# Performance work log

Measured on AMD Instinct MI355X. Metric: run time of the kernel, lower is better.

The kernel has to match this reference:

```python
import jax, jax.numpy as jnp
import numpy as np

INPUT_SIZE = 128
HIDDEN_SIZE = 128
BATCH = 65536


def _xavier(key, shape):
    fan_out, fan_in = shape
    limit = np.sqrt(6.0 / (fan_in + fan_out)).astype(np.float32)
    return jax.random.uniform(key, shape, jnp.float32, -limit, limit)


def setup_inputs() -> dict:
    key = jax.random.key(0)
    ks = jax.random.split(key, 12)
    inp = {
        "x": jax.random.normal(ks[0], (BATCH, INPUT_SIZE), jnp.float32),
        "h_t": jax.random.normal(ks[1], (BATCH, HIDDEN_SIZE), jnp.float32),
        "c_t": jax.random.normal(ks[2], (BATCH, HIDDEN_SIZE), jnp.float32),
        "W_ii": _xavier(ks[3], (HIDDEN_SIZE, INPUT_SIZE)),
        "W_hi": _xavier(ks[4], (HIDDEN_SIZE, HIDDEN_SIZE)),
        "b_i": jnp.zeros((HIDDEN_SIZE,), jnp.float32),
        "W_if": _xavier(ks[5], (HIDDEN_SIZE, INPUT_SIZE)),
        "W_hf": _xavier(ks[6], (HIDDEN_SIZE, HIDDEN_SIZE)),
        "b_f": jnp.zeros((HIDDEN_SIZE,), jnp.float32),
        "W_ig": _xavier(ks[7], (HIDDEN_SIZE, INPUT_SIZE)),
        "W_hg": _xavier(ks[8], (HIDDEN_SIZE, HIDDEN_SIZE)),
        "b_g": jnp.zeros((HIDDEN_SIZE,), jnp.float32),
        "W_io": _xavier(ks[9], (HIDDEN_SIZE, INPUT_SIZE)),
        "W_ho": _xavier(ks[10], (HIDDEN_SIZE, HIDDEN_SIZE)),
        "b_o": jnp.zeros((HIDDEN_SIZE,), jnp.float32),
    }
    return inp


def reference(x, h_t, c_t, W_ii, W_hi, b_i, W_if, W_hf, b_f, W_ig, W_hg, b_g, W_io, W_ho, b_o):
    # Fuse the 8 small GEMMs into 2 concatenated GEMMs, identical math to
    # per-gate F.linear calls (same weights, just stacked along output dim).
    W_x = jnp.concatenate([W_ii, W_if, W_ig, W_io], axis=0)   # [4H, I]
    W_h = jnp.concatenate([W_hi, W_hf, W_hg, W_ho], axis=0)   # [4H, H]
    b = jnp.concatenate([b_i, b_f, b_g, b_o], axis=0)         # [4H]
    gates = x @ W_x.T + h_t @ W_h.T + b                       # [B, 4H]
    i_a, f_a, g_a, o_a = jnp.split(gates, 4, axis=1)
    i_t = jax.nn.sigmoid(i_a)
    f_t = jax.nn.sigmoid(f_a)
    g_t = jnp.tanh(g_a)
    o_t = jax.nn.sigmoid(o_a)
    c_new = f_t * c_t + i_t * g_t
    h_new = o_t * jnp.tanh(c_new)
    return (h_new, c_new)
```

## Files before the change

kernel.cpp:

```cpp
#include <hip/hip_runtime.h>
#include <hip/hip_bf16.h>


typedef short s16x8 __attribute__((ext_vector_type(8)));
typedef float f32x4 __attribute__((ext_vector_type(4)));

__device__ __forceinline__ short f2bf(float f) {
    __hip_bfloat16 h = __float2bfloat16(f);
    return __builtin_bit_cast(short, h);
}
__device__ __forceinline__ float sigm(float x) { return 1.0f / (1.0f + __expf(-x)); }
__device__ __forceinline__ float tanh_f(float x) { return 1.0f - 2.0f / (1.0f + __expf(2.0f * x)); }

__global__ __launch_bounds__(256)
void repack_weights(const float* __restrict__ Wii, const float* __restrict__ Whi,
                    const float* __restrict__ Wif, const float* __restrict__ Whf,
                    const float* __restrict__ Wig, const float* __restrict__ Whg,
                    const float* __restrict__ Wio, const float* __restrict__ Who,
                    short* __restrict__ ws)
{
    const int t     = blockIdx.x * 256 + threadIdx.x;
    const int chunk = t >> 6;
    const int l     = t & 63;
    const int ks    = chunk & 3;
    const int half  = (chunk >> 2) & 1;
    const int g     = (chunk >> 3) & 3;
    const int wn    = (chunk >> 5) & 1;
    const int jt    = chunk >> 6;
    const int j     = jt * 32 + wn * 16 + (l & 15);
    const int k0    = (ks * 4 + (l >> 4)) * 8;

    const float* wp;
    if (half == 0) wp = (g == 0) ? Wii : (g == 1) ? Wif : (g == 2) ? Wig : Wio;
    else           wp = (g == 0) ? Whi : (g == 1) ? Whf : (g == 2) ? Whg : Who;

    const float* src = wp + (size_t)j * 128 + k0;
    f32x4 a = *(const f32x4*)src;
    f32x4 b = *(const f32x4*)(src + 4);
    s16x8 v;
#pragma unroll
    for (int k = 0; k < 4; ++k) { v[k] = f2bf(a[k]); v[4 + k] = f2bf(b[k]); }
    *(s16x8*)(ws + (size_t)t * 8) = v;
}

__global__ __launch_bounds__(256, 3)
void lstm_cell_kernel(const float* __restrict__ X,
                      const float* __restrict__ H,
                      const float* __restrict__ C,
                      const float* __restrict__ Bi, const float* __restrict__ Bf,
                      const float* __restrict__ Bg, const float* __restrict__ Bo,
                      const short* __restrict__ WS,
                      float* __restrict__ OutH,
                      float* __restrict__ OutC)
{
    __shared__ short sA[128 * 128];

    const int tid = threadIdx.x;
    const int l  = tid & 63;
    const int w  = tid >> 6;
    const int wm = w & 1;
    const int wn = w >> 1;
    const int lj = l & 15;
    const int lq = l >> 4;

    const int jt = blockIdx.x & 3;
    const int bb = blockIdx.x >> 2;
    const int B0 = bb * 128;
    const int J0 = jt * 32;

    f32x4 acc[4][4];
#pragma unroll
    for (int mt = 0; mt < 4; ++mt)
#pragma unroll
        for (int g = 0; g < 4; ++g)
            acc[mt][g] = (f32x4){0.f, 0.f, 0.f, 0.f};

    const short* wsbase = WS + ((size_t)(jt * 2 + wn) * 32) * 512 + l * 8;

#pragma unroll
    for (int half = 0; half < 2; ++half) {
        const float* Asrc = half ? H : X;

        s16x8 bfh[4][4];
#pragma unroll
        for (int g = 0; g < 4; ++g)
#pragma unroll
            for (int ks = 0; ks < 4; ++ks)
                bfh[g][ks] = *(const s16x8*)(wsbase + (size_t)((g * 2 + half) * 4 + ks) * 512);

#pragma unroll
        for (int tt = 0; tt < 2; ++tt) {
            f32x4 f[4][2];
#pragma unroll
            for (int t = 0; t < 4; ++t) {
                const int cc   = (tt * 4 + t) * 256 + tid;
                const int m    = cc >> 4;
                const int oct  = cc & 15;
                const int soct = oct ^ (m & 15);
                const float* src = Asrc + (size_t)(B0 + m) * 128 + soct * 8;
                f[t][0] = *(const f32x4*)src;
                f[t][1] = *(const f32x4*)(src + 4);
            }
#pragma unroll
            for (int t = 0; t < 4; ++t) {
                const int cc = (tt * 4 + t) * 256 + tid;
                s16x8 v;
#pragma unroll
                for (int k = 0; k < 4; ++k) {
                    v[k]     = f2bf(f[t][0][k]);
                    v[4 + k] = f2bf(f[t][1][k]);
                }
                *(s16x8*)(sA + cc * 8) = v;
            }
        }
        __syncthreads();

#pragma unroll
        for (int ks = 0; ks < 4; ++ks) {
            const int oct = (ks * 4 + lq) ^ lj;
            s16x8 af[4];
#pragma unroll
            for (int mt = 0; mt < 4; ++mt) {
                const int m = wm * 64 + mt * 16 + lj;
                af[mt] = *(const s16x8*)(sA + m * 128 + oct * 8);
            }
#pragma unroll
            for (int mt = 0; mt < 4; ++mt)
#pragma unroll
                for (int g = 0; g < 4; ++g)
                    acc[mt][g] = __builtin_amdgcn_mfma_f32_16x16x32_bf16(
                        af[mt], bfh[g][ks], acc[mt][g], 0, 0, 0);
        }
        __syncthreads();
    }

    const int j = J0 + wn * 16 + lj;
    const float bi  = Bi[j];
    const float bfv = Bf[j];
    const float bg  = Bg[j];
    const float bo  = Bo[j];

#pragma unroll
    for (int mt = 0; mt < 4; ++mt) {
#pragma unroll
        for (int r = 0; r < 4; ++r) {
            const int b   = B0 + wm * 64 + mt * 16 + lq * 4 + r;
            const size_t idx = (size_t)b * 128 + j;
            const float ia = acc[mt][0][r] + bi;
            const float fa = acc[mt][1][r] + bfv;
            const float ga = acc[mt][2][r] + bg;
            const float oa = acc[mt][3][r] + bo;
            const float it = sigm(ia);
            const float ft = sigm(fa);
            const float gt = tanh_f(ga);
            const float ot = sigm(oa);
            const float co = C[idx];
            const float cn = ft * co + it * gt;
            const float hn = ot * tanh_f(cn);
            OutH[idx] = hn;
            OutC[idx] = cn;
        }
    }
}

extern "C" void kernel_launch(void* const* d_in, const int* in_sizes, int n_in,
                              void* d_out, int out_size, void* d_ws, size_t ws_size,
                              hipStream_t stream) {
    const float* X   = (const float*)d_in[0];
    const float* H   = (const float*)d_in[1];
    const float* C   = (const float*)d_in[2];
    const float* Wii = (const float*)d_in[3];
    const float* Whi = (const float*)d_in[4];
    const float* Bi  = (const float*)d_in[5];
    const float* Wif = (const float*)d_in[6];
    const float* Whf = (const float*)d_in[7];
    const float* Bf  = (const float*)d_in[8];
    const float* Wig = (const float*)d_in[9];
    const float* Whg = (const float*)d_in[10];
    const float* Bg  = (const float*)d_in[11];
    const float* Wio = (const float*)d_in[12];
    const float* Who = (const float*)d_in[13];
    const float* Bo  = (const float*)d_in[14];

    short* ws = (short*)d_ws;

    hipLaunchKernelGGL(repack_weights, dim3(64), dim3(256), 0, stream,
                       Wii, Whi, Wif, Whf, Wig, Whg, Wio, Who, ws);

    float* OutH = (float*)d_out;
    float* OutC = OutH + (size_t)65536 * 128;

    hipLaunchKernelGGL(lstm_cell_kernel, dim3(2048), dim3(256), 0, stream,
                       X, H, C, Bi, Bf, Bg, Bo, ws, OutH, OutC);
}
```

Before: 196.0 us.

## Tile by 32 batch rows with full hidden width and async global-to-LDS loads

Each block now covers 32 batch rows and all 128 hidden columns, so X and H are read from global memory once instead of once per column tile (previously four column tiles each re-read the same rows). The X and H tiles are staged as fp32 in LDS through global_load_lds DMA with an XOR swizzle, and bf16 conversion happens at fragment-read time. Weight fragments are streamed from the repacked workspace, which is read directly from global/L2 inside the k loop, and occupancy is raised to 4 blocks per SM. The tradeoffs are a grid of 2048 small blocks with a single synchronisation point, and more weight traffic per block.

```diff
diff --git a/kernel.cpp b/kernel.cpp
--- a/kernel.cpp
+++ b/kernel.cpp
@@ -12,6 +12,12 @@
 __device__ __forceinline__ float sigm(float x) { return 1.0f / (1.0f + __expf(-x)); }
 __device__ __forceinline__ float tanh_f(float x) { return 1.0f - 2.0f / (1.0f + __expf(2.0f * x)); }
 
+__device__ __forceinline__ void dma16(const float* g, void* lds) {
+    __builtin_amdgcn_global_load_lds(
+        (const __attribute__((address_space(1))) void*)g,
+        (__attribute__((address_space(3))) void*)lds, 16, 0, 0);
+}
+
 __global__ __launch_bounds__(256)
 void repack_weights(const float* __restrict__ Wii, const float* __restrict__ Whi,
                     const float* __restrict__ Wif, const float* __restrict__ Whf,
@@ -19,31 +25,28 @@
                     const float* __restrict__ Wio, const float* __restrict__ Who,
                     short* __restrict__ ws)
 {
-    const int t     = blockIdx.x * 256 + threadIdx.x;
-    const int chunk = t >> 6;
-    const int l     = t & 63;
-    const int ks    = chunk & 3;
-    const int half  = (chunk >> 2) & 1;
-    const int g     = (chunk >> 3) & 3;
-    const int wn    = (chunk >> 5) & 1;
-    const int jt    = chunk >> 6;
-    const int j     = jt * 32 + wn * 16 + (l & 15);
-    const int k0    = (ks * 4 + (l >> 4)) * 8;
+    const int t   = blockIdx.x * 256 + threadIdx.x;
+    const int fi  = t >> 6;
+    const int l   = t & 63;
+    const int ks  = fi & 7;
+    const int g   = (fi >> 3) & 3;
+    const int jt  = fi >> 5;
+    const int j   = jt * 16 + (l & 15);
+    const int k   = ks * 32 + (l >> 4) * 8;
 
-    const float* wp;
-    if (half == 0) wp = (g == 0) ? Wii : (g == 1) ? Wif : (g == 2) ? Wig : Wio;
-    else           wp = (g == 0) ? Whi : (g == 1) ? Whf : (g == 2) ? Whg : Who;
-
-    const float* src = wp + (size_t)j * 128 + k0;
+    const float* wx = (g == 0) ? Wii : (g == 1) ? Wif : (g == 2) ? Wig : Wio;
+    const float* wh = (g == 0) ? Whi : (g == 1) ? Whf : (g == 2) ? Whg : Who;
+    const float* src = (k < 128) ? (wx + (size_t)j * 128 + k)
+                                 : (wh + (size_t)j * 128 + (k - 128));
     f32x4 a = *(const f32x4*)src;
     f32x4 b = *(const f32x4*)(src + 4);
     s16x8 v;
 #pragma unroll
-    for (int k = 0; k < 4; ++k) { v[k] = f2bf(a[k]); v[4 + k] = f2bf(b[k]); }
+    for (int q = 0; q < 4; ++q) { v[q] = f2bf(a[q]); v[4 + q] = f2bf(b[q]); }
     *(s16x8*)(ws + (size_t)t * 8) = v;
 }
 
-__global__ __launch_bounds__(256, 3)
+__global__ __launch_bounds__(256, 4)
 void lstm_cell_kernel(const float* __restrict__ X,
                       const float* __restrict__ H,
                       const float* __restrict__ C,
@@ -53,112 +56,91 @@
                       float* __restrict__ OutH,
                       float* __restrict__ OutC)
 {
-    __shared__ short sA[128 * 128];
+    __shared__ __align__(16) char sA[32768];
 
     const int tid = threadIdx.x;
-    const int l  = tid & 63;
-    const int w  = tid >> 6;
-    const int wm = w & 1;
-    const int wn = w >> 1;
-    const int lj = l & 15;
-    const int lq = l >> 4;
+    const int l   = tid & 63;
+    const int w   = tid >> 6;
+    const int lj  = l & 15;
+    const int lq  = l >> 4;
+    const int B0  = blockIdx.x * 32;
 
-    const int jt = blockIdx.x & 3;
-    const int bb = blockIdx.x >> 2;
-    const int B0 = bb * 128;
-    const int J0 = jt * 32;
+    {
+        const int  ci   = l & 31;
+        const float* base = (l >= 32) ? H : X;
+#pragma unroll
+        for (int r = 0; r < 8; ++r) {
+            const int m = w * 8 + r;
+            const float* src = base + (size_t)(B0 + m) * 128 + ((ci ^ r) << 2);
+            dma16(src, (void*)(sA + m * 1024));
+        }
+    }
 
-    f32x4 acc[4][4];
+    f32x4 acc[2][2][4];
 #pragma unroll
-    for (int mt = 0; mt < 4; ++mt)
+    for (int mt = 0; mt < 2; ++mt)
 #pragma unroll
-        for (int g = 0; g < 4; ++g)
-            acc[mt][g] = (f32x4){0.f, 0.f, 0.f, 0.f};
+        for (int jn = 0; jn < 2; ++jn)
+#pragma unroll
+            for (int g = 0; g < 4; ++g)
+                acc[mt][jn][g] = (f32x4){0.f, 0.f, 0.f, 0.f};
 
-    const short* wsbase = WS + ((size_t)(jt * 2 + wn) * 32) * 512 + l * 8;
+    const short* wsw = WS + (size_t)w * 64 * 512 + l * 8;
+
+    __syncthreads();
 
 #pragma unroll
-    for (int half = 0; half < 2; ++half) {
-        const float* Asrc = half ? H : X;
-
-        s16x8 bfh[4][4];
+    for (int ks = 0; ks < 8; ++ks) {
+        s16x8 af[2];
 #pragma unroll
-        for (int g = 0; g < 4; ++g)
+        for (int mt = 0; mt < 2; ++mt) {
+            const int m  = mt * 16 + lj;
+            const int cg = ks * 8 + lq * 2;
+            const int p0 = (cg & 32) | ((cg & 31) ^ (m & 7));
+            const f32x4 q0 = *(const f32x4*)(sA + m * 1024 + p0 * 16);
+            const f32x4 q1 = *(const f32x4*)(sA + m * 1024 + (p0 ^ 1) * 16);
+            s16x8 v;
 #pragma unroll
-            for (int ks = 0; ks < 4; ++ks)
-                bfh[g][ks] = *(const s16x8*)(wsbase + (size_t)((g * 2 + half) * 4 + ks) * 512);
+            for (int q = 0; q < 4; ++q) { v[q] = f2bf(q0[q]); v[4 + q] = f2bf(q1[q]); }
+            af[mt] = v;
+        }
+#pragma unroll
+        for (int jn = 0; jn < 2; ++jn)
+#pragma unroll
+            for (int g = 0; g < 4; ++g) {
+                const s16x8 bf = *(const s16x8*)(wsw + (size_t)(jn * 32 + g * 8 + ks) * 512);
+                acc[0][jn][g] = __builtin_amdgcn_mfma_f32_16x16x32_bf16(af[0], bf, acc[0][jn][g], 0, 0, 0);
+                acc[1][jn][g] = __builtin_amdgcn_mfma_f32_16x16x32_bf16(af[1], bf, acc[1][jn][g], 0, 0, 0);
+            }
+    }
 
 #pragma unroll
-        for (int tt = 0; tt < 2; ++tt) {
-            f32x4 f[4][2];
+    for (int jn = 0; jn < 2; ++jn) {
+        const int j = w * 32 + jn * 16 + lj;
+        const float bi  = Bi[j];
+        const float bfv = Bf[j];
+        const float bg  = Bg[j];
+        const float bo  = Bo[j];
 #pragma unroll
-            for (int t = 0; t < 4; ++t) {
-                const int cc   = (tt * 4 + t) * 256 + tid;
-                const int m    = cc >> 4;
-                const int oct  = cc & 15;
-                const int soct = oct ^ (m & 15);
-                const float* src = Asrc + (size_t)(B0 + m) * 128 + soct * 8;
-                f[t][0] = *(const f32x4*)src;
-                f[t][1] = *(const f32x4*)(src + 4);
+        for (int mt = 0; mt < 2; ++mt) {
+#pragma unroll
+            for (int r = 0; r < 4; ++r) {
+                const int b = B0 + mt * 16 + lq * 4 + r;
+                const size_t idx = (size_t)b * 128 + j;
+                const float ia = acc[mt][jn][0][r] + bi;
+                const float fa = acc[mt][jn][1][r] + bfv;
+                const float ga = acc[mt][jn][2][r] + bg;
+                const float oa = acc[mt][jn][3][r] + bo;
+                const float it = sigm(ia);
+                const float ft = sigm(fa);
+                const float gt = tanh_f(ga);
+                const float ot = sigm(oa);
+                const float co = C[idx];
+                const float cn = ft * co + it * gt;
+                const float hn = ot * tanh_f(cn);
+                OutH[idx] = hn;
+                OutC[idx] = cn;
             }
-#pragma unroll
-            for (int t = 0; t < 4; ++t) {
-                const int cc = (tt * 4 + t) * 256 + tid;
-                s16x8 v;
-#pragma unroll
-                for (int k = 0; k < 4; ++k) {
-                    v[k]     = f2bf(f[t][0][k]);
-                    v[4 + k] = f2bf(f[t][1][k]);
-                }
-                *(s16x8*)(sA + cc * 8) = v;
-            }
-        }
-        __syncthreads();
-
-#pragma unroll
-        for (int ks = 0; ks < 4; ++ks) {
-            const int oct = (ks * 4 + lq) ^ lj;
-            s16x8 af[4];
-#pragma unroll
-            for (int mt = 0; mt < 4; ++mt) {
-                const int m = wm * 64 + mt * 16 + lj;
-                af[mt] = *(const s16x8*)(sA + m * 128 + oct * 8);
-            }
-#pragma unroll
-            for (int mt = 0; mt < 4; ++mt)
-#pragma unroll
-                for (int g = 0; g < 4; ++g)
-                    acc[mt][g] = __builtin_amdgcn_mfma_f32_16x16x32_bf16(
-                        af[mt], bfh[g][ks], acc[mt][g], 0, 0, 0);
-        }
-        __syncthreads();
-    }
-
-    const int j = J0 + wn * 16 + lj;
-    const float bi  = Bi[j];
-    const float bfv = Bf[j];
-    const float bg  = Bg[j];
-    const float bo  = Bo[j];
-
-#pragma unroll
-    for (int mt = 0; mt < 4; ++mt) {
-#pragma unroll
-        for (int r = 0; r < 4; ++r) {
-            const int b   = B0 + wm * 64 + mt * 16 + lq * 4 + r;
-            const size_t idx = (size_t)b * 128 + j;
-            const float ia = acc[mt][0][r] + bi;
-            const float fa = acc[mt][1][r] + bfv;
-            const float ga = acc[mt][2][r] + bg;
-            const float oa = acc[mt][3][r] + bo;
-            const float it = sigm(ia);
-            const float ft = sigm(fa);
-            const float gt = tanh_f(ga);
-            const float ot = sigm(oa);
-            const float co = C[idx];
-            const float cn = ft * co + it * gt;
-            const float hn = ot * tanh_f(cn);
-            OutH[idx] = hn;
-            OutC[idx] = cn;
         }
     }
 }
```

Result: slower. 226.3 us (+15.5%).
